# Performance work log

Measured on AMD Instinct MI355X. Metric: run time of the kernel, lower is better.

## Reference

```python
import jax, jax.numpy as jnp
import numpy as np

B = 512          # batch
IN_UNITS = 8     # primary capsule dim
IN_CH = 1152     # number of primary capsules
NUM_UNITS = 10   # output capsules (classes)
UNIT_SIZE = 16   # output capsule dim
BETA = 1.45      # squash beta: 1.45 - 0.22*(ep_iter/total) with ep_iter = n_iter = 0
NUM_ROUTING = 3


def setup_inputs() -> dict:
    key = jax.random.key(0)
    k1, k2 = jax.random.split(key)
    x = jax.random.normal(k1, (B, IN_UNITS, IN_CH), dtype=jnp.float32)
    # W parameter: torch shape (1, in_channels, num_units, unit_size, in_units); drop leading 1
    W = jax.random.normal(k2, (IN_CH, NUM_UNITS, UNIT_SIZE, IN_UNITS), dtype=jnp.float32)
    return {"x": x, "W": W}


def _squash(s):
    # s: (B, num_units, unit_size). Torch squash sums dim=2 of (B,1,nu,us,1),
    # which is the num_units axis (axis=1 here). Faithful to source.
    mag_sq = jnp.sum(s * s, axis=1, keepdims=True)          # (B,1,us)
    mag = jnp.sqrt(mag_sq)
    return mag_sq / (BETA + mag_sq) * (s / mag)


def reference(x, W):
    # u_hat[b,i,j,u] = sum_k W[i,j,u,k] * x[b,k,i]
    u_hat = jnp.einsum('ijuk,bki->biju', W, x)               # (B, IN_CH, NUM_UNITS, UNIT_SIZE)
    b_ij = jnp.zeros((IN_CH, NUM_UNITS), dtype=x.dtype)
    v = None
    for _ in range(NUM_ROUTING):
        c = jax.nn.softmax(b_ij, axis=0)                     # softmax over in_channels (dim=1 in torch)
        s = jnp.einsum('ij,biju->bju', c, u_hat)             # (B, NUM_UNITS, UNIT_SIZE)
        v = _squash(s)
        # b update: agreement <u_hat, v>, averaged over batch
        b_ij = jnp.einsum('biju,bju->ij', u_hat, v) / u_hat.shape[0]
    # rearrange 'b c (g h) w -> b c g (h w)' with g=4, w=1 -> reshape (B, nu, 4, us//4)
    return v.reshape(v.shape[0], NUM_UNITS, 4, UNIT_SIZE // 4)
```

## Files before the change

kernel.cpp:

```cpp
#include <hip/hip_runtime.h>
#include <hip/hip_bf16.h>
#include <math.h>

#define B    512
#define INU  8
#define IC   1152
#define NU   10
#define US   16
#define JU   160
#define KI   9216
#define BETAC 1.45f
#define NSPLIT 32
#define KC 288

typedef __attribute__((ext_vector_type(8))) __bf16 bf16x8;
typedef __attribute__((ext_vector_type(4))) float floatx4;

static __device__ __forceinline__ unsigned short f2bf(float f) {
  unsigned u = __builtin_bit_cast(unsigned, f);
  u = (u + 0x7fffu + ((u >> 16) & 1u)) >> 16;
  return (unsigned short)u;
}
static __device__ __forceinline__ float bf2f(unsigned short h) {
  return __builtin_bit_cast(float, ((unsigned)h) << 16);
}
static __device__ __forceinline__ uint4 scale8(uint4 wv, float4 cA, float4 cB) {
  union { uint4 u; unsigned short s[8]; } in;
  in.u = wv;
  union { uint4 u; __hip_bfloat162 h[4]; } o;
  o.h[0] = __float22bfloat162_rn(make_float2(bf2f(in.s[0]) * cA.x, bf2f(in.s[1]) * cA.y));
  o.h[1] = __float22bfloat162_rn(make_float2(bf2f(in.s[2]) * cA.z, bf2f(in.s[3]) * cA.w));
  o.h[2] = __float22bfloat162_rn(make_float2(bf2f(in.s[4]) * cB.x, bf2f(in.s[5]) * cB.y));
  o.h[3] = __float22bfloat162_rn(make_float2(bf2f(in.s[6]) * cB.z, bf2f(in.s[7]) * cB.w));
  return o.u;
}

__global__ __launch_bounds__(256) void prep_kernel(
    const float* __restrict__ x, const float* __restrict__ W,
    unsigned short* __restrict__ xb, unsigned short* __restrict__ xT,
    unsigned short* __restrict__ Wt, unsigned short* __restrict__ Wc,
    float* __restrict__ Wr) {
  __shared__ float ts[32 * 322];
  int id = blockIdx.x;
  int t = threadIdx.x;
  if (id < 1152) {
    int k0 = (id % 144) * 64;
    int b0 = (id / 144) * 64;
#pragma unroll
    for (int r = 0; r < 16; ++r) {
      int idx = t + 256 * r;
      int br = idx >> 6, kc = idx & 63;
      float v = x[(size_t)(b0 + br) * KI + k0 + kc];
      ts[br * 65 + kc] = v;
      xb[(size_t)(b0 + br) * KI + k0 + kc] = f2bf(v);
    }
    __syncthreads();
#pragma unroll
    for (int r = 0; r < 8; ++r) {
      int idx = t + 256 * r;
      int kr = idx >> 5, bc = (idx & 31) * 2;
      unsigned lo = f2bf(ts[bc * 65 + kr]);
      unsigned hi = f2bf(ts[(bc + 1) * 65 + kr]);
      *(unsigned*)&xT[(size_t)(k0 + kr) * B + b0 + bc] = lo | (hi << 16);
    }
  } else {
    int wid = id - 1152;
    int i0 = (wid >> 2) * 32;
    int c0 = (wid & 3) * 320;
#pragma unroll
    for (int r = 0; r < 20; ++r) {
      int q = t + 256 * r;
      int il = q / 160, c = (q - il * 160) * 2;
      *(float2*)&ts[il * 322 + c] =
          *(const float2*)&W[(size_t)(i0 + il) * 1280 + c0 + c];
    }
    __syncthreads();
    {
      const float cinv = 1.0f / (float)IC;
      int il2 = (t & 15) * 2;
      for (int p = (t >> 4); p < 320; p += 16) {
        int c = c0 + p;
        int ju = c >> 3, k = c & 7;
        unsigned lo = f2bf(ts[il2 * 322 + p]);
        unsigned hi = f2bf(ts[(il2 + 1) * 322 + p]);
        *(unsigned*)&Wt[(size_t)ju * KI + k * IC + i0 + il2] = lo | (hi << 16);
        unsigned lo2 = f2bf(bf2f((unsigned short)lo) * cinv);
        unsigned hi2 = f2bf(bf2f((unsigned short)hi) * cinv);
        *(unsigned*)&Wc[(size_t)ju * KI + k * IC + i0 + il2] = lo2 | (hi2 << 16);
      }
    }
    int ju0 = c0 >> 3;
    for (int q = t; q < 8 * 32 * 40; q += 256) {
      int k = q / 1280;
      int il = (q / 40) & 31;
      int jl = q - (q / 40) * 40;
      Wr[((size_t)k * IC + i0 + il) * JU + ju0 + jl] = ts[il * 322 + jl * 8 + k];
    }
  }
}

__global__ __launch_bounds__(256) void s_gemm_mfma(
    const unsigned short* __restrict__ xb, const unsigned short* __restrict__ Wc,
    float* __restrict__ sp) {
  int b0 = blockIdx.x * 64;
  int kbase = blockIdx.y * KC;
  int t = threadIdx.x;
  int w = t >> 6, lane = t & 63, col = lane & 15, quad = lane >> 4;
  __shared__ unsigned short xs[2][64 * 40];
  __shared__ unsigned short ms[2][160 * 40];

  int xrow = t >> 2, xc = (t & 3) * 8;
  int mrow0 = t >> 2, mrow1 = (t + 256) >> 2, mrow2 = (t + 512) >> 2;
  int mc = (t & 3) * 8;

  uint4 xv, m0, m1, m2;
  auto prefetch = [&](int k0) {
    xv = *(const uint4*)&xb[(size_t)(b0 + xrow) * KI + k0 + xc];
    m0 = *(const uint4*)&Wc[(size_t)mrow0 * KI + k0 + mc];
    m1 = *(const uint4*)&Wc[(size_t)mrow1 * KI + k0 + mc];
    if (t < 128) m2 = *(const uint4*)&Wc[(size_t)mrow2 * KI + k0 + mc];
  };
  auto commit = [&](int pb) {
    *(uint4*)&xs[pb][xrow * 40 + xc] = xv;
    *(uint4*)&ms[pb][mrow0 * 40 + mc] = m0;
    *(uint4*)&ms[pb][mrow1 * 40 + mc] = m1;
    if (t < 128) *(uint4*)&ms[pb][mrow2 * 40 + mc] = m2;
  };
  floatx4 acc[10];
#pragma unroll
  for (int jt = 0; jt < 10; ++jt) acc[jt] = (floatx4){0.f, 0.f, 0.f, 0.f};
  const int nsteps = KC >> 5;
  prefetch(kbase);
  commit(0);
  prefetch(kbase + 32);
  for (int s = 0; s < nsteps; ++s) {
    __syncthreads();
    if (s + 1 < nsteps) commit((s + 1) & 1);
    if (s + 2 < nsteps) prefetch(kbase + (s + 2) * 32);
    bf16x8 a = *(bf16x8*)&xs[s & 1][(w * 16 + col) * 40 + quad * 8];
#pragma unroll
    for (int jt = 0; jt < 10; ++jt) {
      bf16x8 bb = *(bf16x8*)&ms[s & 1][(jt * 16 + col) * 40 + quad * 8];
      acc[jt] = __builtin_amdgcn_mfma_f32_16x16x32_bf16(a, bb, acc[jt], 0, 0, 0);
    }
  }
#pragma unroll
  for (int jt = 0; jt < 10; ++jt)
#pragma unroll
    for (int r = 0; r < 4; ++r) {
      int b = b0 + w * 16 + quad * 4 + r;
      sp[((size_t)blockIdx.y * B + b) * JU + jt * 16 + col] = acc[jt][r];
    }
}

__global__ __launch_bounds__(192) void squash_kernel(
    const float* __restrict__ sp, unsigned short* __restrict__ vT,
    float* __restrict__ out) {
  int b = blockIdx.x;
  int t = threadIdx.x;
  __shared__ float sv[JU];
  __shared__ float fac[US];
  float s = 0.0f;
  if (t < JU) {
#pragma unroll
    for (int k = 0; k < NSPLIT; ++k) s += sp[((size_t)k * B + b) * JU + t];
    sv[t] = s;
  }
  __syncthreads();
  if (t < US) {
    float m = 0.0f;
#pragma unroll
    for (int j = 0; j < NU; ++j) {
      float q = sv[j * US + t];
      m += q * q;
    }
    fac[t] = sqrtf(m) / (BETAC + m);
  }
  __syncthreads();
  if (t < JU) {
    float val = s * fac[t & 15];
    vT[(size_t)t * B + b] = f2bf(val);
    if (out) out[(size_t)b * JU + t] = val;
  }
}

__global__ __launch_bounds__(256) void b_update_mfma(
    const unsigned short* __restrict__ xT, const unsigned short* __restrict__ vT,
    const float* __restrict__ Wr, float* __restrict__ bp) {
  int k = blockIdx.x / 18;
  int i0 = (blockIdx.x - k * 18) * 64;
  int bs = blockIdx.y;
  size_t ki0 = (size_t)k * IC + i0;
  int t = threadIdx.x;
  int w = t >> 6, lane = t & 63, col = lane & 15, quad = lane >> 4;
  __shared__ unsigned short xs[2][64 * 40];
  __shared__ unsigned short vs[2][160 * 40];
  int xrow = t >> 2, xc = (t & 3) * 8;
  int mrow0 = t >> 2, mrow1 = (t + 256) >> 2, mrow2 = (t + 512) >> 2;
  int mc = (t & 3) * 8;
  uint4 xv, m0, m1, m2;
  auto prefetch = [&](int c0) {
    xv = *(const uint4*)&xT[(ki0 + xrow) * B + c0 + xc];
    m0 = *(const uint4*)&vT[(size_t)mrow0 * B + c0 + mc];
    m1 = *(const uint4*)&vT[(size_t)mrow1 * B + c0 + mc];
    if (t < 128) m2 = *(const uint4*)&vT[(size_t)mrow2 * B + c0 + mc];
  };
  auto commit = [&](int pb) {
    *(uint4*)&xs[pb][xrow * 40 + xc] = xv;
    *(uint4*)&vs[pb][mrow0 * 40 + mc] = m0;
    *(uint4*)&vs[pb][mrow1 * 40 + mc] = m1;
    if (t < 128) *(uint4*)&vs[pb][mrow2 * 40 + mc] = m2;
  };
  floatx4 acc[10];
#pragma unroll
  for (int jt = 0; jt < 10; ++jt) acc[jt] = (floatx4){0.f, 0.f, 0.f, 0.f};
  prefetch(bs * 256);
  commit(0);
  prefetch(bs * 256 + 32);
  for (int s = 0; s < 8; ++s) {
    __syncthreads();
    if (s + 1 < 8) commit((s + 1) & 1);
    if (s + 2 < 8) prefetch(bs * 256 + (s + 2) * 32);
    bf16x8 a = *(bf16x8*)&xs[s & 1][(w * 16 + col) * 40 + quad * 8];
#pragma unroll
    for (int jt = 0; jt < 10; ++jt) {
      bf16x8 bb = *(bf16x8*)&vs[s & 1][(jt * 16 + col) * 40 + quad * 8];
      acc[jt] = __builtin_amdgcn_mfma_f32_16x16x32_bf16(a, bb, acc[jt], 0, 0, 0);
    }
  }
  int p = k * 2 + bs;
#pragma unroll
  for (int jt = 0; jt < 10; ++jt) {
#pragma unroll
    for (int r = 0; r < 4; ++r) {
      int i = i0 + w * 16 + quad * 4 + r;
      float wv = Wr[((size_t)k * IC + i) * JU + jt * 16 + col];
      float pr = wv * acc[jt][r];
      pr += __shfl_xor(pr, 1);
      pr += __shfl_xor(pr, 2);
      pr += __shfl_xor(pr, 4);
      pr += __shfl_xor(pr, 8);
      if (col == 0)
        bp[(size_t)p * (IC * NU) + jt * IC + i] = pr * (1.0f / (float)B);
    }
  }
}

__global__ __launch_bounds__(256) void softmax_scale_kernel(
    const float* __restrict__ bp, const unsigned short* __restrict__ Wt,
    unsigned short* __restrict__ Wc) {
  int ju = blockIdx.x;
  int j = ju >> 4;
  int t = threadIdx.x;
  __shared__ float c[IC];
  __shared__ float red[256];
  for (int i = t; i < IC; i += 256) {
    float s = 0.0f;
#pragma unroll
    for (int p = 0; p < 16; ++p) s += bp[(size_t)p * (IC * NU) + j * IC + i];
    c[i] = s;
  }
  __syncthreads();
  float m = -1e30f;
  for (int i = t; i < IC; i += 256) m = fmaxf(m, c[i]);
  red[t] = m;
  __syncthreads();
  for (int o = 128; o > 0; o >>= 1) {
    if (t < o) red[t] = fmaxf(red[t], red[t + o]);
    __syncthreads();
  }
  float mx = red[0];
  __syncthreads();
  float sm = 0.0f;
  for (int i = t; i < IC; i += 256) {
    float e = __expf(c[i] - mx);
    c[i] = e;
    sm += e;
  }
  red[t] = sm;
  __syncthreads();
  for (int o = 128; o > 0; o >>= 1) {
    if (t < o) red[t] += red[t + o];
    __syncthreads();
  }
  float inv = 1.0f / red[0];
  for (int q = t; q < KI / 8; q += 256) {
    int ki = q * 8;
    int i = ki % IC;
    uint4 wv = *(const uint4*)&Wt[(size_t)ju * KI + ki];
    float4 cA = make_float4(c[i] * inv, c[i + 1] * inv, c[i + 2] * inv, c[i + 3] * inv);
    float4 cB = make_float4(c[i + 4] * inv, c[i + 5] * inv, c[i + 6] * inv, c[i + 7] * inv);
    *(uint4*)&Wc[(size_t)ju * KI + ki] = scale8(wv, cA, cB);
  }
}

extern "C" void kernel_launch(void* const* d_in, const int* in_sizes, int n_in,
                              void* d_out, int out_size, void* d_ws,
                              size_t ws_size, hipStream_t stream) {
  const float* x = (const float*)d_in[0];
  const float* W = (const float*)d_in[1];
  float* out = (float*)d_out;

  char* pws = (char*)d_ws;
  float* bp = (float*)pws;                     pws += (size_t)16 * IC * NU * 4;
  float* sp = (float*)pws;                     pws += (size_t)NSPLIT * B * JU * 4;
  float* Wr = (float*)pws;                     pws += (size_t)KI * JU * 4;
  unsigned short* xb = (unsigned short*)pws;   pws += (size_t)B * KI * 2;
  unsigned short* xT = (unsigned short*)pws;   pws += (size_t)KI * B * 2;
  unsigned short* Wt = (unsigned short*)pws;   pws += (size_t)JU * KI * 2;
  unsigned short* Wc = (unsigned short*)pws;   pws += (size_t)JU * KI * 2;
  unsigned short* vT = (unsigned short*)pws;

  prep_kernel<<<1152 + 144, 256, 0, stream>>>(x, W, xb, xT, Wt, Wc, Wr);

  for (int it = 0; it < 3; ++it) {
    s_gemm_mfma<<<dim3(8, NSPLIT), 256, 0, stream>>>(xb, Wc, sp);
    squash_kernel<<<B, 192, 0, stream>>>(sp, vT, (it == 2) ? out : nullptr);
    if (it < 2) {
      b_update_mfma<<<dim3(144, 2), 256, 0, stream>>>(xT, vT, Wr, bp);
      softmax_scale_kernel<<<160, 256, 0, stream>>>(bp, Wt, Wc);
    }
  }
}
```

Baseline: 171.9 us.

## Fuse routing iterations into one persistent kernel with grid-wide barriers

Replaces the per-iteration launches of the s-GEMM, squash, b-update and softmax-scale kernels with a single persistent routing kernel of 256 blocks. The stages are separated by a software grid barrier built on an atomic counter that the prep kernel resets. This removes roughly ten kernel launches and their launch gaps. In exchange it relies on all 256 blocks being co-resident, since otherwise the spin barrier deadlocks. The b-update stage is also load-balanced over 288 work items on 256 blocks, which gives it a partial second wave.

```diff
diff --git a/kernel.cpp b/kernel.cpp
--- a/kernel.cpp
+++ b/kernel.cpp
@@ -39,10 +39,11 @@
     const float* __restrict__ x, const float* __restrict__ W,
     unsigned short* __restrict__ xb, unsigned short* __restrict__ xT,
     unsigned short* __restrict__ Wt, unsigned short* __restrict__ Wc,
-    float* __restrict__ Wr) {
+    float* __restrict__ Wr, int* __restrict__ gbar) {
   __shared__ float ts[32 * 322];
   int id = blockIdx.x;
   int t = threadIdx.x;
+  if (id == 0 && t == 0) *gbar = 0;
   if (id < 1152) {
     int k0 = (id % 144) * 64;
     int b0 = (id / 144) * 64;
@@ -99,198 +100,216 @@
   }
 }
 
-__global__ __launch_bounds__(256) void s_gemm_mfma(
-    const unsigned short* __restrict__ xb, const unsigned short* __restrict__ Wc,
-    float* __restrict__ sp) {
-  int b0 = blockIdx.x * 64;
-  int kbase = blockIdx.y * KC;
-  int t = threadIdx.x;
-  int w = t >> 6, lane = t & 63, col = lane & 15, quad = lane >> 4;
-  __shared__ unsigned short xs[2][64 * 40];
-  __shared__ unsigned short ms[2][160 * 40];
-
-  int xrow = t >> 2, xc = (t & 3) * 8;
-  int mrow0 = t >> 2, mrow1 = (t + 256) >> 2, mrow2 = (t + 512) >> 2;
-  int mc = (t & 3) * 8;
-
-  uint4 xv, m0, m1, m2;
-  auto prefetch = [&](int k0) {
-    xv = *(const uint4*)&xb[(size_t)(b0 + xrow) * KI + k0 + xc];
-    m0 = *(const uint4*)&Wc[(size_t)mrow0 * KI + k0 + mc];
-    m1 = *(const uint4*)&Wc[(size_t)mrow1 * KI + k0 + mc];
-    if (t < 128) m2 = *(const uint4*)&Wc[(size_t)mrow2 * KI + k0 + mc];
+__global__ __launch_bounds__(256) void routing_kernel(
+    const unsigned short* __restrict__ xb, const unsigned short* __restrict__ xT,
+    const unsigned short* __restrict__ Wt, unsigned short* __restrict__ Wc,
+    const float* __restrict__ Wr, float* __restrict__ sp,
+    unsigned short* __restrict__ vT, float* __restrict__ bp,
+    float* __restrict__ out, int* __restrict__ gbar) {
+  __shared__ uint4 smem4[35840 / 16];
+  unsigned short* xs = (unsigned short*)smem4;
+  unsigned short* ms = (unsigned short*)((char*)smem4 + 10240);
+  float* c_sh = (float*)smem4;
+  float* red  = (float*)((char*)smem4 + IC * 4);
+  float* sv   = (float*)smem4;
+  float* fac  = (float*)((char*)smem4 + JU * 4);
+
+  const int t = threadIdx.x;
+  const int w = t >> 6, lane = t & 63, col = lane & 15, quad = lane >> 4;
+  const int xrow = t >> 2, xc = (t & 3) * 8;
+  const int mrow0 = t >> 2, mrow1 = (t + 256) >> 2, mrow2 = (t + 512) >> 2;
+  const int mc = (t & 3) * 8;
+
+  int barg = 0;
+  auto gsync = [&]() {
+    ++barg;
+    __syncthreads();
+    if (t == 0) {
+      __threadfence();
+      __hip_atomic_fetch_add(gbar, 1, __ATOMIC_RELAXED, __HIP_MEMORY_SCOPE_AGENT);
+      while (__hip_atomic_load(gbar, __ATOMIC_RELAXED, __HIP_MEMORY_SCOPE_AGENT) <
+             barg * 256)
+        __builtin_amdgcn_s_sleep(2);
+      __threadfence();
+    }
+    __syncthreads();
   };
-  auto commit = [&](int pb) {
-    *(uint4*)&xs[pb][xrow * 40 + xc] = xv;
-    *(uint4*)&ms[pb][mrow0 * 40 + mc] = m0;
-    *(uint4*)&ms[pb][mrow1 * 40 + mc] = m1;
-    if (t < 128) *(uint4*)&ms[pb][mrow2 * 40 + mc] = m2;
-  };
-  floatx4 acc[10];
-#pragma unroll
-  for (int jt = 0; jt < 10; ++jt) acc[jt] = (floatx4){0.f, 0.f, 0.f, 0.f};
-  const int nsteps = KC >> 5;
-  prefetch(kbase);
-  commit(0);
-  prefetch(kbase + 32);
-  for (int s = 0; s < nsteps; ++s) {
-    __syncthreads();
-    if (s + 1 < nsteps) commit((s + 1) & 1);
-    if (s + 2 < nsteps) prefetch(kbase + (s + 2) * 32);
-    bf16x8 a = *(bf16x8*)&xs[s & 1][(w * 16 + col) * 40 + quad * 8];
-#pragma unroll
-    for (int jt = 0; jt < 10; ++jt) {
-      bf16x8 bb = *(bf16x8*)&ms[s & 1][(jt * 16 + col) * 40 + quad * 8];
-      acc[jt] = __builtin_amdgcn_mfma_f32_16x16x32_bf16(a, bb, acc[jt], 0, 0, 0);
-    }
-  }
-#pragma unroll
-  for (int jt = 0; jt < 10; ++jt)
-#pragma unroll
-    for (int r = 0; r < 4; ++r) {
-      int b = b0 + w * 16 + quad * 4 + r;
-      sp[((size_t)blockIdx.y * B + b) * JU + jt * 16 + col] = acc[jt][r];
-    }
-}
-
-__global__ __launch_bounds__(192) void squash_kernel(
-    const float* __restrict__ sp, unsigned short* __restrict__ vT,
-    float* __restrict__ out) {
-  int b = blockIdx.x;
-  int t = threadIdx.x;
-  __shared__ float sv[JU];
-  __shared__ float fac[US];
-  float s = 0.0f;
-  if (t < JU) {
-#pragma unroll
-    for (int k = 0; k < NSPLIT; ++k) s += sp[((size_t)k * B + b) * JU + t];
-    sv[t] = s;
-  }
-  __syncthreads();
-  if (t < US) {
-    float m = 0.0f;
-#pragma unroll
-    for (int j = 0; j < NU; ++j) {
-      float q = sv[j * US + t];
-      m += q * q;
-    }
-    fac[t] = sqrtf(m) / (BETAC + m);
-  }
-  __syncthreads();
-  if (t < JU) {
-    float val = s * fac[t & 15];
-    vT[(size_t)t * B + b] = f2bf(val);
-    if (out) out[(size_t)b * JU + t] = val;
-  }
-}
-
-__global__ __launch_bounds__(256) void b_update_mfma(
-    const unsigned short* __restrict__ xT, const unsigned short* __restrict__ vT,
-    const float* __restrict__ Wr, float* __restrict__ bp) {
-  int k = blockIdx.x / 18;
-  int i0 = (blockIdx.x - k * 18) * 64;
-  int bs = blockIdx.y;
-  size_t ki0 = (size_t)k * IC + i0;
-  int t = threadIdx.x;
-  int w = t >> 6, lane = t & 63, col = lane & 15, quad = lane >> 4;
-  __shared__ unsigned short xs[2][64 * 40];
-  __shared__ unsigned short vs[2][160 * 40];
-  int xrow = t >> 2, xc = (t & 3) * 8;
-  int mrow0 = t >> 2, mrow1 = (t + 256) >> 2, mrow2 = (t + 512) >> 2;
-  int mc = (t & 3) * 8;
-  uint4 xv, m0, m1, m2;
-  auto prefetch = [&](int c0) {
-    xv = *(const uint4*)&xT[(ki0 + xrow) * B + c0 + xc];
-    m0 = *(const uint4*)&vT[(size_t)mrow0 * B + c0 + mc];
-    m1 = *(const uint4*)&vT[(size_t)mrow1 * B + c0 + mc];
-    if (t < 128) m2 = *(const uint4*)&vT[(size_t)mrow2 * B + c0 + mc];
-  };
-  auto commit = [&](int pb) {
-    *(uint4*)&xs[pb][xrow * 40 + xc] = xv;
-    *(uint4*)&vs[pb][mrow0 * 40 + mc] = m0;
-    *(uint4*)&vs[pb][mrow1 * 40 + mc] = m1;
-    if (t < 128) *(uint4*)&vs[pb][mrow2 * 40 + mc] = m2;
-  };
-  floatx4 acc[10];
-#pragma unroll
-  for (int jt = 0; jt < 10; ++jt) acc[jt] = (floatx4){0.f, 0.f, 0.f, 0.f};
-  prefetch(bs * 256);
-  commit(0);
-  prefetch(bs * 256 + 32);
-  for (int s = 0; s < 8; ++s) {
-    __syncthreads();
-    if (s + 1 < 8) commit((s + 1) & 1);
-    if (s + 2 < 8) prefetch(bs * 256 + (s + 2) * 32);
-    bf16x8 a = *(bf16x8*)&xs[s & 1][(w * 16 + col) * 40 + quad * 8];
-#pragma unroll
-    for (int jt = 0; jt < 10; ++jt) {
-      bf16x8 bb = *(bf16x8*)&vs[s & 1][(jt * 16 + col) * 40 + quad * 8];
-      acc[jt] = __builtin_amdgcn_mfma_f32_16x16x32_bf16(a, bb, acc[jt], 0, 0, 0);
-    }
-  }
-  int p = k * 2 + bs;
-#pragma unroll
-  for (int jt = 0; jt < 10; ++jt) {
-#pragma unroll
-    for (int r = 0; r < 4; ++r) {
-      int i = i0 + w * 16 + quad * 4 + r;
-      float wv = Wr[((size_t)k * IC + i) * JU + jt * 16 + col];
-      float pr = wv * acc[jt][r];
-      pr += __shfl_xor(pr, 1);
-      pr += __shfl_xor(pr, 2);
-      pr += __shfl_xor(pr, 4);
-      pr += __shfl_xor(pr, 8);
-      if (col == 0)
-        bp[(size_t)p * (IC * NU) + jt * IC + i] = pr * (1.0f / (float)B);
-    }
-  }
-}
-
-__global__ __launch_bounds__(256) void softmax_scale_kernel(
-    const float* __restrict__ bp, const unsigned short* __restrict__ Wt,
-    unsigned short* __restrict__ Wc) {
-  int ju = blockIdx.x;
-  int j = ju >> 4;
-  int t = threadIdx.x;
-  __shared__ float c[IC];
-  __shared__ float red[256];
-  for (int i = t; i < IC; i += 256) {
-    float s = 0.0f;
-#pragma unroll
-    for (int p = 0; p < 16; ++p) s += bp[(size_t)p * (IC * NU) + j * IC + i];
-    c[i] = s;
-  }
-  __syncthreads();
-  float m = -1e30f;
-  for (int i = t; i < IC; i += 256) m = fmaxf(m, c[i]);
-  red[t] = m;
-  __syncthreads();
-  for (int o = 128; o > 0; o >>= 1) {
-    if (t < o) red[t] = fmaxf(red[t], red[t + o]);
-    __syncthreads();
-  }
-  float mx = red[0];
-  __syncthreads();
-  float sm = 0.0f;
-  for (int i = t; i < IC; i += 256) {
-    float e = __expf(c[i] - mx);
-    c[i] = e;
-    sm += e;
-  }
-  red[t] = sm;
-  __syncthreads();
-  for (int o = 128; o > 0; o >>= 1) {
-    if (t < o) red[t] += red[t + o];
-    __syncthreads();
-  }
-  float inv = 1.0f / red[0];
-  for (int q = t; q < KI / 8; q += 256) {
-    int ki = q * 8;
-    int i = ki % IC;
-    uint4 wv = *(const uint4*)&Wt[(size_t)ju * KI + ki];
-    float4 cA = make_float4(c[i] * inv, c[i + 1] * inv, c[i + 2] * inv, c[i + 3] * inv);
-    float4 cB = make_float4(c[i + 4] * inv, c[i + 5] * inv, c[i + 6] * inv, c[i + 7] * inv);
-    *(uint4*)&Wc[(size_t)ju * KI + ki] = scale8(wv, cA, cB);
+
+  for (int it = 0; it < 3; ++it) {
+    {
+      const int b0 = (blockIdx.x & 7) * 64;
+      const int kbase = (blockIdx.x >> 3) * KC;
+      uint4 xv, m0, m1, m2;
+      auto prefetch = [&](int k0) {
+        xv = *(const uint4*)&xb[(size_t)(b0 + xrow) * KI + k0 + xc];
+        m0 = *(const uint4*)&Wc[(size_t)mrow0 * KI + k0 + mc];
+        m1 = *(const uint4*)&Wc[(size_t)mrow1 * KI + k0 + mc];
+        if (t < 128) m2 = *(const uint4*)&Wc[(size_t)mrow2 * KI + k0 + mc];
+      };
+      auto commit = [&](int pb) {
+        *(uint4*)&xs[pb * 2560 + xrow * 40 + xc] = xv;
+        *(uint4*)&ms[pb * 6400 + mrow0 * 40 + mc] = m0;
+        *(uint4*)&ms[pb * 6400 + mrow1 * 40 + mc] = m1;
+        if (t < 128) *(uint4*)&ms[pb * 6400 + mrow2 * 40 + mc] = m2;
+      };
+      floatx4 acc[10];
+#pragma unroll
+      for (int jt = 0; jt < 10; ++jt) acc[jt] = (floatx4){0.f, 0.f, 0.f, 0.f};
+      const int nsteps = KC >> 5;
+      prefetch(kbase);
+      commit(0);
+      prefetch(kbase + 32);
+      for (int s = 0; s < nsteps; ++s) {
+        __syncthreads();
+        if (s + 1 < nsteps) commit((s + 1) & 1);
+        if (s + 2 < nsteps) prefetch(kbase + (s + 2) * 32);
+        bf16x8 a = *(bf16x8*)&xs[(s & 1) * 2560 + (w * 16 + col) * 40 + quad * 8];
+#pragma unroll
+        for (int jt = 0; jt < 10; ++jt) {
+          bf16x8 bb = *(bf16x8*)&ms[(s & 1) * 6400 + (jt * 16 + col) * 40 + quad * 8];
+          acc[jt] = __builtin_amdgcn_mfma_f32_16x16x32_bf16(a, bb, acc[jt], 0, 0, 0);
+        }
+      }
+#pragma unroll
+      for (int jt = 0; jt < 10; ++jt)
+#pragma unroll
+        for (int r = 0; r < 4; ++r) {
+          int b = b0 + w * 16 + quad * 4 + r;
+          sp[((size_t)(blockIdx.x >> 3) * B + b) * JU + jt * 16 + col] = acc[jt][r];
+        }
+    }
+    gsync();
+
+    for (int bi = 0; bi < 2; ++bi) {
+      int b = blockIdx.x * 2 + bi;
+      float s = 0.0f;
+      if (t < JU) {
+#pragma unroll
+        for (int k = 0; k < NSPLIT; ++k) s += sp[((size_t)k * B + b) * JU + t];
+        sv[t] = s;
+      }
+      __syncthreads();
+      if (t < US) {
+        float m = 0.0f;
+#pragma unroll
+        for (int j = 0; j < NU; ++j) {
+          float q = sv[j * US + t];
+          m += q * q;
+        }
+        fac[t] = sqrtf(m) / (BETAC + m);
+      }
+      __syncthreads();
+      if (t < JU) {
+        float val = s * fac[t & 15];
+        vT[(size_t)t * B + b] = f2bf(val);
+        if (it == 2) out[(size_t)b * JU + t] = val;
+      }
+      __syncthreads();
+    }
+    if (it == 2) return;
+    gsync();
+
+    for (int item = blockIdx.x; item < 288; item += gridDim.x) {
+      const int bu = item >> 1;
+      const int bs = item & 1;
+      const int k = bu / 18;
+      const int i0 = (bu - k * 18) * 64;
+      const size_t ki0 = (size_t)k * IC + i0;
+      __syncthreads();
+      uint4 xv, m0, m1, m2;
+      auto prefetch = [&](int c0) {
+        xv = *(const uint4*)&xT[(ki0 + xrow) * B + c0 + xc];
+        m0 = *(const uint4*)&vT[(size_t)mrow0 * B + c0 + mc];
+        m1 = *(const uint4*)&vT[(size_t)mrow1 * B + c0 + mc];
+        if (t < 128) m2 = *(const uint4*)&vT[(size_t)mrow2 * B + c0 + mc];
+      };
+      auto commit = [&](int pb) {
+        *(uint4*)&xs[pb * 2560 + xrow * 40 + xc] = xv;
+        *(uint4*)&ms[pb * 6400 + mrow0 * 40 + mc] = m0;
+        *(uint4*)&ms[pb * 6400 + mrow1 * 40 + mc] = m1;
+        if (t < 128) *(uint4*)&ms[pb * 6400 + mrow2 * 40 + mc] = m2;
+      };
+      floatx4 acc[10];
+#pragma unroll
+      for (int jt = 0; jt < 10; ++jt) acc[jt] = (floatx4){0.f, 0.f, 0.f, 0.f};
+      prefetch(bs * 256);
+      commit(0);
+      prefetch(bs * 256 + 32);
+      for (int s = 0; s < 8; ++s) {
+        __syncthreads();
+        if (s + 1 < 8) commit((s + 1) & 1);
+        if (s + 2 < 8) prefetch(bs * 256 + (s + 2) * 32);
+        bf16x8 a = *(bf16x8*)&xs[(s & 1) * 2560 + (w * 16 + col) * 40 + quad * 8];
+#pragma unroll
+        for (int jt = 0; jt < 10; ++jt) {
+          bf16x8 bb = *(bf16x8*)&ms[(s & 1) * 6400 + (jt * 16 + col) * 40 + quad * 8];
+          acc[jt] = __builtin_amdgcn_mfma_f32_16x16x32_bf16(a, bb, acc[jt], 0, 0, 0);
+        }
+      }
+      const int p = k * 2 + bs;
+#pragma unroll
+      for (int jt = 0; jt < 10; ++jt) {
+#pragma unroll
+        for (int r = 0; r < 4; ++r) {
+          int i = i0 + w * 16 + quad * 4 + r;
+          float wv = Wr[((size_t)k * IC + i) * JU + jt * 16 + col];
+          float pr = wv * acc[jt][r];
+          pr += __shfl_xor(pr, 1);
+          pr += __shfl_xor(pr, 2);
+          pr += __shfl_xor(pr, 4);
+          pr += __shfl_xor(pr, 8);
+          if (col == 0)
+            bp[(size_t)p * (IC * NU) + jt * IC + i] = pr * (1.0f / (float)B);
+        }
+      }
+    }
+    gsync();
+
+    if (blockIdx.x < 160) {
+      const int ju = blockIdx.x;
+      const int j = ju >> 4;
+      for (int i = t; i < IC; i += 256) {
+        float s = 0.0f;
+#pragma unroll
+        for (int p = 0; p < 16; ++p) s += bp[(size_t)p * (IC * NU) + j * IC + i];
+        c_sh[i] = s;
+      }
+      __syncthreads();
+      float m = -1e30f;
+      for (int i = t; i < IC; i += 256) m = fmaxf(m, c_sh[i]);
+      red[t] = m;
+      __syncthreads();
+      for (int o = 128; o > 0; o >>= 1) {
+        if (t < o) red[t] = fmaxf(red[t], red[t + o]);
+        __syncthreads();
+      }
+      float mx = red[0];
+      __syncthreads();
+      float sm = 0.0f;
+      for (int i = t; i < IC; i += 256) {
+        float e = __expf(c_sh[i] - mx);
+        c_sh[i] = e;
+        sm += e;
+      }
+      red[t] = sm;
+      __syncthreads();
+      for (int o = 128; o > 0; o >>= 1) {
+        if (t < o) red[t] += red[t + o];
+        __syncthreads();
+      }
+      float inv = 1.0f / red[0];
+      for (int q = t; q < KI / 8; q += 256) {
+        int ki = q * 8;
+        int i = ki % IC;
+        uint4 wv = *(const uint4*)&Wt[(size_t)ju * KI + ki];
+        float4 cA = make_float4(c_sh[i] * inv, c_sh[i + 1] * inv,
+                                c_sh[i + 2] * inv, c_sh[i + 3] * inv);
+        float4 cB = make_float4(c_sh[i + 4] * inv, c_sh[i + 5] * inv,
+                                c_sh[i + 6] * inv, c_sh[i + 7] * inv);
+        *(uint4*)&Wc[(size_t)ju * KI + ki] = scale8(wv, cA, cB);
+      }
+    }
+    gsync();
   }
 }
 
@@ -309,16 +328,10 @@
   unsigned short* xT = (unsigned short*)pws;   pws += (size_t)KI * B * 2;
   unsigned short* Wt = (unsigned short*)pws;   pws += (size_t)JU * KI * 2;
   unsigned short* Wc = (unsigned short*)pws;   pws += (size_t)JU * KI * 2;
-  unsigned short* vT = (unsigned short*)pws;
-
-  prep_kernel<<<1152 + 144, 256, 0, stream>>>(x, W, xb, xT, Wt, Wc, Wr);
-
-  for (int it = 0; it < 3; ++it) {
-    s_gemm_mfma<<<dim3(8, NSPLIT), 256, 0, stream>>>(xb, Wc, sp);
-    squash_kernel<<<B, 192, 0, stream>>>(sp, vT, (it == 2) ? out : nullptr);
-    if (it < 2) {
-      b_update_mfma<<<dim3(144, 2), 256, 0, stream>>>(xT, vT, Wr, bp);
-      softmax_scale_kernel<<<160, 256, 0, stream>>>(bp, Wt, Wc);
-    }
-  }
-}
+  unsigned short* vT = (unsigned short*)pws;   pws += (size_t)JU * B * 2;
+  int* gbar = (int*)pws;
+
+  prep_kernel<<<1152 + 144, 256, 0, stream>>>(x, W, xb, xT, Wt, Wc, Wr, gbar);
+  routing_kernel<<<256, 256, 0, stream>>>(xb, xT, Wt, Wc, Wr, sp, vT, bp, out,
+                                          gbar);
+}
```

Result: slower. 400.5 us (+133.0%).
